# Optimization experiments

Measured on AMD Instinct MI355X. Metric: run time of the kernel, lower is better.

Reference implementation:

```python
import jax, jax.numpy as jnp
import numpy as np

B, C, H, W = 32, 256, 32, 32
HEADS, DH = 8, 32          # MHA9: num_heads=8, dim_head=32, total_dim=256
TOT = HEADS * DH


def setup_inputs() -> dict:
    key = jax.random.key(0)
    ks = jax.random.split(key, 10)
    s = 0.02
    return {
        "x": jax.random.normal(ks[0], (B, C, H, W), dtype=jnp.float32),
        "Wq": jax.random.normal(ks[1], (TOT, C), dtype=jnp.float32) * s,
        "bq": jnp.zeros((TOT,), dtype=jnp.float32),
        "Wk": jax.random.normal(ks[2], (TOT, C), dtype=jnp.float32) * s,
        "bk": jnp.zeros((TOT,), dtype=jnp.float32),
        "Wv": jax.random.normal(ks[3], (TOT, C), dtype=jnp.float32) * s,
        "bv": jnp.zeros((TOT,), dtype=jnp.float32),
        "Wo": jax.random.normal(ks[4], (C, TOT), dtype=jnp.float32) * s,
        "bo": jnp.zeros((C,), dtype=jnp.float32),
        "gamma": jnp.zeros((1,), dtype=jnp.float32),
    }


def reference(x, Wq, bq, Wk, bk, Wv, bv, Wo, bo, gamma):
    b, c, h, w = x.shape
    S = h * w

    def proj(Wt, bt):
        # 1x1 conv == channel matmul; reshape to (B, heads, S, dh)
        y = jnp.einsum('oc,bchw->bohw', Wt, x) + bt[None, :, None, None]
        return y.reshape(b, HEADS, DH, S).transpose(0, 1, 3, 2)

    q = proj(Wq, bq)
    k = proj(Wk, bk)
    v = proj(Wv, bv)

    scale = 1.0 / jnp.sqrt(jnp.asarray(DH, dtype=x.dtype))
    scores = jnp.einsum('bhsd,bhtd->bhst', q, k) * scale  # [B,h,S,S] full matrix
    weights = jax.nn.softmax(scores, axis=-1)
    o = jnp.einsum('bhst,bhtd->bhsd', weights, v)          # [B,h,S,dh]
    o = o.transpose(0, 1, 3, 2).reshape(b, TOT, h, w)
    o = jnp.einsum('oc,bchw->bohw', Wo, o) + bo[None, :, None, None]
    x_ = gamma * o + x   # inner residual of MultiHeadAttention
    return x + x_        # outer residual of MulAttontion
```

## Files before the change

### kernel.cpp

```cpp
#include <hip/hip_runtime.h>
#include <stdint.h>

typedef unsigned short u16;
typedef unsigned int   u32;
typedef __attribute__((ext_vector_type(8))) short bf16x8;
typedef __attribute__((ext_vector_type(4))) short bf16x4;
typedef __attribute__((ext_vector_type(4))) float f32x4;
typedef __attribute__((ext_vector_type(16))) float f32x16;

#define NT ((size_t)8388608)

__device__ __forceinline__ float bf2f(u16 u) {
  union { float f; u32 i; } v; v.i = ((u32)u) << 16; return v.f;
}
__device__ __forceinline__ u16 f2bf(float f) {
  union { float f; u32 i; } v; v.f = f;
  u32 r = (v.i + 0x7fffu + ((v.i >> 16) & 1u)) >> 16;
  return (u16)r;
}
__device__ __forceinline__ u32 fbits(float f) {
  union { float f; u32 i; } v; v.f = f; return v.i;
}
__device__ __forceinline__ int detect_bf16(const u32* __restrict__ xd) {
  u32 w = xd[threadIdx.x & 63];
  u32 e = (w >> 8) & 0x7fu;
  unsigned long long m = __ballot((e >= 0x38u) && (e <= 0x41u));
  return __popcll(m) > 32;
}
__device__ __forceinline__ void gld16(const void* g, void* l) {
  __builtin_amdgcn_global_load_lds((const __attribute__((address_space(1))) u32*)g,
                                   (__attribute__((address_space(3))) u32*)l, 16, 0, 0);
}

__global__ void __launch_bounds__(256) prologue_kernel(const void* __restrict__ xin,
                                                       u16* __restrict__ xT,
                                                       const void* __restrict__ W0, const void* __restrict__ W1,
                                                       const void* __restrict__ W2, const void* __restrict__ b0,
                                                       const void* __restrict__ b1, const void* __restrict__ b2,
                                                       u16* __restrict__ wdst, float* __restrict__ bdst,
                                                       const void* __restrict__ Wo, const void* __restrict__ bo,
                                                       const void* __restrict__ gm, u16* __restrict__ wodst,
                                                       float* __restrict__ bodst) {
  const int blk = blockIdx.x;
  const int tid = threadIdx.x;
  const int isbf = detect_bf16((const u32*)xin);
  if (blk < 2048) {
    const int s0 = (blk & 15) * 64, c0 = ((blk >> 4) & 3) * 64, b = blk >> 6;
    __shared__ u16 T[64][72];
    if (isbf) {
      const u16* xp = (const u16*)xin;
      for (int t = tid; t < 512; t += 256) {
        int r = t >> 3, off = (t & 7) * 8;
        *(uint4*)&T[r][off] = *(const uint4*)(xp + ((size_t)(b * 256 + c0 + r)) * 1024 + s0 + off);
      }
    } else {
      const float* xp = (const float*)xin;
      for (int t = tid; t < 512; t += 256) {
        int r = t >> 3, off = (t & 7) * 8;
        const float* s = xp + ((size_t)(b * 256 + c0 + r)) * 1024 + s0 + off;
#pragma unroll
        for (int u = 0; u < 8; u++) T[r][off + u] = f2bf(s[u]);
      }
    }
    __syncthreads();
    for (int t = tid; t < 512; t += 256) {
      int r = t >> 3, off = (t & 7) * 8;
      union { u16 h[8]; uint4 v; } pk;
#pragma unroll
      for (int u = 0; u < 8; u++) pk.h[u] = T[off + u][r];
      *(uint4*)(xT + ((size_t)(b * 1024 + s0 + r)) * 256 + c0 + off) = pk.v;
    }
  } else if (blk < 2240) {
    const int g = blk - 2048;
    const int which = g >> 6, bk = g & 63;
    const void* Ws = which == 0 ? W0 : which == 1 ? W1 : W2;
    const void* bs = which == 0 ? b0 : which == 1 ? b1 : b2;
    const int idx = bk * 1024 + tid * 4;
    u16* dst = wdst + which * 65536 + idx;
    if (isbf) {
      *(ushort4*)dst = *(const ushort4*)((const u16*)Ws + idx);
    } else {
      const float* s = (const float*)Ws + idx;
      ushort4 o; o.x = f2bf(s[0]); o.y = f2bf(s[1]); o.z = f2bf(s[2]); o.w = f2bf(s[3]);
      *(ushort4*)dst = o;
    }
    if (bk == 0) {
      bdst[which * 256 + tid] = isbf ? bf2f(((const u16*)bs)[tid]) : ((const float*)bs)[tid];
    }
  } else {
    const int g = blk - 2240;
    const int idx = g * 1024 + tid * 4;
    if (isbf) {
      *(ushort4*)(wodst + idx) = *(const ushort4*)((const u16*)Wo + idx);
    } else {
      const float* s = (const float*)Wo + idx;
      ushort4 o; o.x = f2bf(s[0]); o.y = f2bf(s[1]); o.z = f2bf(s[2]); o.w = f2bf(s[3]);
      *(ushort4*)(wodst + idx) = o;
    }
    if (g == 0) {
      bodst[tid] = isbf ? bf2f(((const u16*)bo)[tid]) : ((const float*)bo)[tid];
      if (tid == 0) bodst[256] = isbf ? bf2f(((const u16*)gm)[0]) : ((const float*)gm)[0];
    }
  }
}

__global__ void __launch_bounds__(256) prep_o(const void* __restrict__ Wo, const void* __restrict__ bo,
                                              const void* __restrict__ gm, u16* __restrict__ wdst,
                                              float* __restrict__ bdst, const u32* __restrict__ xdet) {
  const int isbf = detect_bf16(xdet);
  const int idx = blockIdx.x * 1024 + threadIdx.x * 4;
  if (isbf) {
    *(ushort4*)(wdst + idx) = *(const ushort4*)((const u16*)Wo + idx);
  } else {
    const float* s = (const float*)Wo + idx;
    ushort4 o; o.x = f2bf(s[0]); o.y = f2bf(s[1]); o.z = f2bf(s[2]); o.w = f2bf(s[3]);
    *(ushort4*)(wdst + idx) = o;
  }
  if (blockIdx.x == 0) {
    int t = threadIdx.x;
    bdst[t] = isbf ? bf2f(((const u16*)bo)[t]) : ((const float*)bo)[t];
    if (t == 0) bdst[256] = isbf ? bf2f(((const u16*)gm)[0]) : ((const float*)gm)[0];
  }
}

__global__ void __launch_bounds__(256) qkv_gemm(const u16* __restrict__ xT,
                                                const u16* __restrict__ Wall,
                                                const float* __restrict__ ball,
                                                u16* __restrict__ Qb, u16* __restrict__ Kb,
                                                u16* __restrict__ Vb) {
  const int z = blockIdx.z, b = z / 3, which = z - b * 3;
  const int tid = threadIdx.x, lane = tid & 63, wave = tid >> 6;
  const int quad = lane >> 4, l16 = lane & 15;
  const int wm = wave >> 1, wn = wave & 1;
  const u16* xb = xT + (size_t)b * 262144;
  const u16* W = Wall + which * 65536;
  int m0, n0; const u16 *Abase, *Bbase;
  if (which < 2) { m0 = blockIdx.y * 128; n0 = blockIdx.x * 128; Abase = xb; Bbase = W; }
  else           { m0 = blockIdx.x * 128; n0 = blockIdx.y * 128; Abase = W; Bbase = xb; }

  __shared__ u16 Ash[8192], Bsh[8192];
  f32x4 acc[4][4];
#pragma unroll
  for (int i = 0; i < 4; i++)
#pragma unroll
    for (int j = 0; j < 4; j++) acc[i][j] = (f32x4){0.f, 0.f, 0.f, 0.f};

  const int srow = lane >> 3, scol = (lane & 7) * 8;
  for (int k0 = 0; k0 < 256; k0 += 64) {
    __syncthreads();
#pragma unroll
    for (int p = 0; p < 4; p++) {
      const int row = p * 32 + wave * 8;
      gld16(Abase + (size_t)(m0 + row + srow) * 256 + k0 + scol, &Ash[row * 64 + lane * 8]);
      gld16(Bbase + (size_t)(n0 + row + srow) * 256 + k0 + scol, &Bsh[row * 64 + lane * 8]);
    }
    __syncthreads();
#pragma unroll
    for (int kk = 0; kk < 2; kk++) {
      bf16x8 av[4], bv[4];
#pragma unroll
      for (int i = 0; i < 4; i++) av[i] = *(const bf16x8*)&Ash[(wm * 64 + i * 16 + l16) * 64 + kk * 32 + quad * 8];
#pragma unroll
      for (int j = 0; j < 4; j++) bv[j] = *(const bf16x8*)&Bsh[(wn * 64 + j * 16 + l16) * 64 + kk * 32 + quad * 8];
#pragma unroll
      for (int i = 0; i < 4; i++)
#pragma unroll
        for (int j = 0; j < 4; j++)
          acc[i][j] = __builtin_amdgcn_mfma_f32_16x16x32_bf16(av[i], bv[j], acc[i][j], 0, 0, 0);
    }
  }

  const float* bias = ball + which * 256;
  const float scale = (which == 0) ? 0.25503486f : 1.0f;
#pragma unroll
  for (int i = 0; i < 4; i++) {
#pragma unroll
    for (int j = 0; j < 4; j++) {
      const int mb = m0 + wm * 64 + i * 16 + quad * 4;
      const int n = n0 + wn * 64 + j * 16 + l16;
#pragma unroll
      for (int r = 0; r < 4; r++) {
        const int m = mb + r;
        float v = acc[i][j][r];
        if (which < 2) {
          v = (v + bias[n]) * scale;
          u16* D = (which ? Kb : Qb) + (size_t)b * 262144;
          D[(size_t)m * 256 + n] = f2bf(v);
        } else {
          v = v + bias[m];
          (Vb + (size_t)b * 262144)[(size_t)m * 1024 + n] = f2bf(v);
        }
      }
    }
  }
}

__global__ void __launch_bounds__(512, 4) attn_kernel(const u16* __restrict__ Q,
                                                      const u16* __restrict__ K,
                                                      const u16* __restrict__ V,
                                                      u16* __restrict__ O) {
  const int blk = blockIdx.x;
  const int qc = blk >> 8, bh = blk & 255;
  const int b = bh >> 3, h = bh & 7;
  const int tid = threadIdx.x, wave = tid >> 6, lane = tid & 63;
  const int hi = lane >> 5, l32 = lane & 31;
  __shared__ __align__(16) u16 Ksh[2][128 * 32];
  __shared__ __align__(16) u16 Vsh[2][32 * 128];
  const u16* Qg = Q + (size_t)b * 262144 + h * 32;
  const u16* Kg = K + (size_t)b * 262144 + h * 32;
  const u16* Vg = V + (size_t)b * 262144 + (size_t)h * 32768;
  const int qw = qc * 256 + wave * 32;

  bf16x8 qf[2];
#pragma unroll
  for (int ks = 0; ks < 2; ks++)
    qf[ks] = *(const bf16x8*)(Qg + (size_t)(qw + l32) * 256 + ks * 16 + hi * 8);

  const int Gg = wave * 64 + lane;
  const int th = Gg >> 3;
  const int uu = (Gg & 7) ^ (th & 7);
  const u16* ksrc = Kg + (size_t)(th * 2 + (uu >> 2)) * 256 + (uu & 3) * 8;
  u16* kdst0 = &Ksh[0][Gg * 8];
  u16* kdst1 = &Ksh[1][Gg * 8];
  const int vd = tid >> 4;
  const u16* vsrc = Vg + (size_t)vd * 1024 + ((tid & 15) ^ (vd & 15)) * 8;
  u16* vdst0 = &Vsh[0][tid * 8];
  u16* vdst1 = &Vsh[1][tid * 8];

  const int kkey = (l32 >> 1) & 7;
  const int kb0 = (l32 >> 1) * 128 + (((((l32 & 1) << 2) | 0 | hi) ^ kkey) << 4);
  const int kb1 = (l32 >> 1) * 128 + (((((l32 & 1) << 2) | 2 | hi) ^ kkey) << 4);
  int vb[4];
#pragma unroll
  for (int tt = 0; tt < 4; tt++) vb[tt] = l32 * 256 + (((l32 & 12) ^ (tt << 2)) << 4);
  const int vm0 = ((l32 & 3) ^ hi) << 4;
  const int vm1 = ((l32 & 3) ^ (2 | hi)) << 4;

  f32x16 oacc;
#pragma unroll
  for (int r = 0; r < 16; r++) oacc[r] = 0.f;
  float lsum = 0.f;

  gld16(ksrc, kdst0);
  gld16(vsrc, vdst0);
  __syncthreads();

#pragma unroll 1
  for (int kt = 0; kt < 8; kt++) {
    const int c = kt & 1;
    if (kt < 7) {
      gld16(ksrc + (size_t)(kt + 1) * 32768, c ? kdst0 : kdst1);
      gld16(vsrc + (kt + 1) * 128,           c ? vdst0 : vdst1);
    }
    const char* Kb = (const char*)&Ksh[c][0];
    const char* Vb = (const char*)&Vsh[c][0];
#pragma unroll
    for (int tt = 0; tt < 4; tt++) {
      const bf16x8 kf0 = *(const bf16x8*)(Kb + tt * 2048 + kb0);
      const bf16x8 kf1 = *(const bf16x8*)(Kb + tt * 2048 + kb1);
      const bf16x8 vf0 = *(const bf16x8*)(Vb + vb[tt] + vm0);
      const bf16x8 vf1 = *(const bf16x8*)(Vb + vb[tt] + vm1);
      f32x16 sf;
#pragma unroll
      for (int r = 0; r < 16; r++) sf[r] = 0.f;
      __builtin_amdgcn_s_setprio(1);
      sf = __builtin_amdgcn_mfma_f32_32x32x16_bf16(kf0, qf[0], sf, 0, 0, 0);
      sf = __builtin_amdgcn_mfma_f32_32x32x16_bf16(kf1, qf[1], sf, 0, 0, 0);
      __builtin_amdgcn_s_setprio(0);
      {
        const float p0 = __builtin_amdgcn_exp2f(sf[0]);
        const float p1 = __builtin_amdgcn_exp2f(sf[1]);
        const float p2 = __builtin_amdgcn_exp2f(sf[2]);
        const float p3 = __builtin_amdgcn_exp2f(sf[3]);
        const float p4 = __builtin_amdgcn_exp2f(sf[4]);
        const float p5 = __builtin_amdgcn_exp2f(sf[5]);
        const float p6 = __builtin_amdgcn_exp2f(sf[6]);
        const float p7 = __builtin_amdgcn_exp2f(sf[7]);
        lsum += ((p0 + p1) + (p2 + p3)) + ((p4 + p5) + (p6 + p7));
        u32 wa, wb, wc, wd;
        asm("v_cvt_pk_bf16_f32 %0, %1, %2" : "=v"(wa) : "v"(p0), "v"(p1));
        asm("v_cvt_pk_bf16_f32 %0, %1, %2" : "=v"(wb) : "v"(p2), "v"(p3));
        asm("v_cvt_pk_bf16_f32 %0, %1, %2" : "=v"(wc) : "v"(p4), "v"(p5));
        asm("v_cvt_pk_bf16_f32 %0, %1, %2" : "=v"(wd) : "v"(p6), "v"(p7));
#if __has_builtin(__builtin_amdgcn_permlane32_swap)
        auto s0 = __builtin_amdgcn_permlane32_swap((int)wc, (int)wa, false, false);
        auto s1 = __builtin_amdgcn_permlane32_swap((int)wd, (int)wb, false, false);
        union { int w[4]; bf16x8 v; } pk;
        pk.w[0] = s0[1]; pk.w[1] = s1[1]; pk.w[2] = s0[0]; pk.w[3] = s1[0];
#else
        const u32 xa = __shfl_xor((int)wa, 32), xb = __shfl_xor((int)wb, 32);
        const u32 xc = __shfl_xor((int)wc, 32), xd = __shfl_xor((int)wd, 32);
        union { u32 w[4]; bf16x8 v; } pk;
        pk.w[0] = hi ? xc : wa; pk.w[1] = hi ? xd : wb;
        pk.w[2] = hi ? wc : xa; pk.w[3] = hi ? wd : xb;
#endif
        __builtin_amdgcn_s_setprio(1);
        oacc = __builtin_amdgcn_mfma_f32_32x32x16_bf16(pk.v, vf0, oacc, 0, 0, 0);
        __builtin_amdgcn_s_setprio(0);
      }
      {
        const float p0 = __builtin_amdgcn_exp2f(sf[8]);
        const float p1 = __builtin_amdgcn_exp2f(sf[9]);
        const float p2 = __builtin_amdgcn_exp2f(sf[10]);
        const float p3 = __builtin_amdgcn_exp2f(sf[11]);
        const float p4 = __builtin_amdgcn_exp2f(sf[12]);
        const float p5 = __builtin_amdgcn_exp2f(sf[13]);
        const float p6 = __builtin_amdgcn_exp2f(sf[14]);
        const float p7 = __builtin_amdgcn_exp2f(sf[15]);
        lsum += ((p0 + p1) + (p2 + p3)) + ((p4 + p5) + (p6 + p7));
        u32 wa, wb, wc, wd;
        asm("v_cvt_pk_bf16_f32 %0, %1, %2" : "=v"(wa) : "v"(p0), "v"(p1));
        asm("v_cvt_pk_bf16_f32 %0, %1, %2" : "=v"(wb) : "v"(p2), "v"(p3));
        asm("v_cvt_pk_bf16_f32 %0, %1, %2" : "=v"(wc) : "v"(p4), "v"(p5));
        asm("v_cvt_pk_bf16_f32 %0, %1, %2" : "=v"(wd) : "v"(p6), "v"(p7));
#if __has_builtin(__builtin_amdgcn_permlane32_swap)
        auto s0 = __builtin_amdgcn_permlane32_swap((int)wc, (int)wa, false, false);
        auto s1 = __builtin_amdgcn_permlane32_swap((int)wd, (int)wb, false, false);
        union { int w[4]; bf16x8 v; } pk;
        pk.w[0] = s0[1]; pk.w[1] = s1[1]; pk.w[2] = s0[0]; pk.w[3] = s1[0];
#else
        const u32 xa = __shfl_xor((int)wa, 32), xb = __shfl_xor((int)wb, 32);
        const u32 xc = __shfl_xor((int)wc, 32), xd = __shfl_xor((int)wd, 32);
        union { u32 w[4]; bf16x8 v; } pk;
        pk.w[0] = hi ? xc : wa; pk.w[1] = hi ? xd : wb;
        pk.w[2] = hi ? wc : xa; pk.w[3] = hi ? wd : xb;
#endif
        __builtin_amdgcn_s_setprio(1);
        oacc = __builtin_amdgcn_mfma_f32_32x32x16_bf16(pk.v, vf1, oacc, 0, 0, 0);
        __builtin_amdgcn_s_setprio(0);
      }
    }
    if (kt < 7) __syncthreads();
  }

  lsum += __shfl_xor(lsum, 32);
  const float linv = 1.0f / lsum;
  u16* Og = O + (size_t)(b * 1024 + qw) * 256 + h * 32 + l32;
#pragma unroll
  for (int r = 0; r < 16; r++) {
    const int qo = (r & 3) + 8 * (r >> 2) + 4 * hi;
    const float li = __shfl(linv, qo);
    Og[(size_t)qo * 256] = f2bf(oacc[r] * li);
  }
}

__global__ void __launch_bounds__(256) out_gemm(const u16* __restrict__ WoB,
                                                const float* __restrict__ bg,
                                                const u16* __restrict__ Ob,
                                                const void* __restrict__ xin,
                                                void* __restrict__ outp,
                                                const u32* __restrict__ xdet) {
  const int b = blockIdx.z;
  const int m0 = blockIdx.y * 128, n0 = blockIdx.x * 128;
  const int tid = threadIdx.x, lane = tid & 63, wave = tid >> 6;
  const int quad = lane >> 4, l16 = lane & 15;
  const int wm = wave >> 1, wn = wave & 1;
  const int isbf = detect_bf16(xdet);
  const u16* Bb = Ob + (size_t)b * 262144;
  __shared__ u16 Ash[8192], Bsh[8192];
  f32x4 acc[4][4];
#pragma unroll
  for (int i = 0; i < 4; i++)
#pragma unroll
    for (int j = 0; j < 4; j++) acc[i][j] = (f32x4){0.f, 0.f, 0.f, 0.f};

  const int srow = lane >> 3, scol = (lane & 7) * 8;
  for (int k0 = 0; k0 < 256; k0 += 64) {
    __syncthreads();
#pragma unroll
    for (int p = 0; p < 4; p++) {
      const int row = p * 32 + wave * 8;
      gld16(WoB + (size_t)(m0 + row + srow) * 256 + k0 + scol, &Ash[row * 64 + lane * 8]);
      gld16(Bb  + (size_t)(n0 + row + srow) * 256 + k0 + scol, &Bsh[row * 64 + lane * 8]);
    }
    __syncthreads();
#pragma unroll
    for (int kk = 0; kk < 2; kk++) {
      bf16x8 av[4], bv[4];
#pragma unroll
      for (int i = 0; i < 4; i++) av[i] = *(const bf16x8*)&Ash[(wm * 64 + i * 16 + l16) * 64 + kk * 32 + quad * 8];
#pragma unroll
      for (int j = 0; j < 4; j++) bv[j] = *(const bf16x8*)&Bsh[(wn * 64 + j * 16 + l16) * 64 + kk * 32 + quad * 8];
#pragma unroll
      for (int i = 0; i < 4; i++)
#pragma unroll
        for (int j = 0; j < 4; j++)
          acc[i][j] = __builtin_amdgcn_mfma_f32_16x16x32_bf16(av[i], bv[j], acc[i][j], 0, 0, 0);
    }
  }

  const float g = bg[256];
#pragma unroll
  for (int i = 0; i < 4; i++) {
#pragma unroll
    for (int j = 0; j < 4; j++) {
      const int mb = m0 + wm * 64 + i * 16 + quad * 4;
      const int n = n0 + wn * 64 + j * 16 + l16;
#pragma unroll
      for (int r = 0; r < 4; r++) {
        const int m = mb + r;
        const float v = acc[i][j][r] + bg[m];
        const size_t gi = (size_t)b * 262144 + (size_t)m * 1024 + n;
        const float xv = isbf ? bf2f(((const u16*)xin)[gi]) : ((const float*)xin)[gi];
        const float res = 2.f * xv + g * v;
        if (isbf) ((u16*)outp)[gi] = f2bf(res);
        else      ((float*)outp)[gi] = res;
      }
    }
  }
}

extern "C" void kernel_launch(void* const* d_in, const int* in_sizes, int n_in,
                              void* d_out, int out_size, void* d_ws, size_t ws_size,
                              hipStream_t stream) {
  const void* x  = d_in[0];
  const void* Wq = d_in[1]; const void* bq = d_in[2];
  const void* Wk = d_in[3]; const void* bk = d_in[4];
  const void* Wv = d_in[5]; const void* bv = d_in[6];
  const void* Wo = d_in[7]; const void* bo = d_in[8];
  const void* gm = d_in[9];

  u16* ws = (u16*)d_ws;
  u16* xT = ws;
  u16* Qb = ws + NT;
  u16* Kb = ws + 2 * NT;
  u16* Vb = ws + 3 * NT;
  u16* Ob = xT;
  const u32* xdet = (const u32*)x;

  u16* WqkvB = (u16*)d_out;
  float* bqkvF = (float*)((u16*)d_out + 196608);

  const bool tail = ws_size >= (size_t)(4 * NT + 66048) * 2;
  u16* WoB = tail ? (ws + 4 * NT) : Qb;
  float* boF = tail ? (float*)(ws + 4 * NT + 65536) : (float*)(Qb + 65536);

  prologue_kernel<<<dim3(tail ? 2304 : 2240), 256, 0, stream>>>(
      x, xT, Wq, Wk, Wv, bq, bk, bv, WqkvB, bqkvF, Wo, bo, gm, WoB, boF);
  qkv_gemm<<<dim3(2, 8, 96), 256, 0, stream>>>(xT, WqkvB, bqkvF, Qb, Kb, Vb);
  attn_kernel<<<dim3(1024), 512, 0, stream>>>(Qb, Kb, Vb, Ob);
  if (!tail) prep_o<<<dim3(64), 256, 0, stream>>>(Wo, bo, gm, WoB, boF, xdet);
  out_gemm<<<dim3(8, 2, 32), 256, 0, stream>>>(WoB, boF, Ob, x, d_out, xdet);
}
```

Before: 210.5 us.

## Swizzle GEMM LDS tiles, shrink out_gemm M-tile, pin attention waves per EU

Applies an XOR swizzle to the LDS column groups in both qkv_gemm and out_gemm so the 16-byte MFMA operand reads avoid bank conflicts. out_gemm's M tile is halved from 128 to 64, doubling its grid for more parallelism on the 256-CU device at the cost of more B-tile reloads. The attention kernel now sets occupancy through the amdgpu_waves_per_eu(4,4) attribute, and its per-iteration zero-init of the score accumulator is replaced by a hoisted zero vector.

```diff
diff --git a/kernel.cpp b/kernel.cpp
--- a/kernel.cpp
+++ b/kernel.cpp
@@ -145,23 +145,25 @@
 #pragma unroll
     for (int j = 0; j < 4; j++) acc[i][j] = (f32x4){0.f, 0.f, 0.f, 0.f};
 
-  const int srow = lane >> 3, scol = (lane & 7) * 8;
+  const int srow = lane >> 3;
+  const int sgc = (lane & 7) ^ (srow & 7);
   for (int k0 = 0; k0 < 256; k0 += 64) {
     __syncthreads();
 #pragma unroll
     for (int p = 0; p < 4; p++) {
       const int row = p * 32 + wave * 8;
-      gld16(Abase + (size_t)(m0 + row + srow) * 256 + k0 + scol, &Ash[row * 64 + lane * 8]);
-      gld16(Bbase + (size_t)(n0 + row + srow) * 256 + k0 + scol, &Bsh[row * 64 + lane * 8]);
+      gld16(Abase + (size_t)(m0 + row + srow) * 256 + k0 + sgc * 8, &Ash[row * 64 + lane * 8]);
+      gld16(Bbase + (size_t)(n0 + row + srow) * 256 + k0 + sgc * 8, &Bsh[row * 64 + lane * 8]);
     }
     __syncthreads();
 #pragma unroll
     for (int kk = 0; kk < 2; kk++) {
       bf16x8 av[4], bv[4];
-#pragma unroll
-      for (int i = 0; i < 4; i++) av[i] = *(const bf16x8*)&Ash[(wm * 64 + i * 16 + l16) * 64 + kk * 32 + quad * 8];
-#pragma unroll
-      for (int j = 0; j < 4; j++) bv[j] = *(const bf16x8*)&Bsh[(wn * 64 + j * 16 + l16) * 64 + kk * 32 + quad * 8];
+      const int rg = (kk * 4 + quad) ^ (l16 & 7);
+#pragma unroll
+      for (int i = 0; i < 4; i++) av[i] = *(const bf16x8*)&Ash[(wm * 64 + i * 16 + l16) * 64 + rg * 8];
+#pragma unroll
+      for (int j = 0; j < 4; j++) bv[j] = *(const bf16x8*)&Bsh[(wn * 64 + j * 16 + l16) * 64 + rg * 8];
 #pragma unroll
       for (int i = 0; i < 4; i++)
 #pragma unroll
@@ -195,10 +197,12 @@
   }
 }
 
-__global__ void __launch_bounds__(512, 4) attn_kernel(const u16* __restrict__ Q,
-                                                      const u16* __restrict__ K,
-                                                      const u16* __restrict__ V,
-                                                      u16* __restrict__ O) {
+__global__ void __launch_bounds__(512)
+__attribute__((amdgpu_waves_per_eu(4, 4)))
+attn_kernel(const u16* __restrict__ Q,
+            const u16* __restrict__ K,
+            const u16* __restrict__ V,
+            u16* __restrict__ O) {
   const int blk = blockIdx.x;
   const int qc = blk >> 8, bh = blk & 255;
   const int b = bh >> 3, h = bh & 7;
@@ -239,6 +243,9 @@
   f32x16 oacc;
 #pragma unroll
   for (int r = 0; r < 16; r++) oacc[r] = 0.f;
+  f32x16 zro;
+#pragma unroll
+  for (int r = 0; r < 16; r++) zro[r] = 0.f;
   float lsum = 0.f;
 
   gld16(ksrc, kdst0);
@@ -260,11 +267,8 @@
       const bf16x8 kf1 = *(const bf16x8*)(Kb + tt * 2048 + kb1);
       const bf16x8 vf0 = *(const bf16x8*)(Vb + vb[tt] + vm0);
       const bf16x8 vf1 = *(const bf16x8*)(Vb + vb[tt] + vm1);
-      f32x16 sf;
-#pragma unroll
-      for (int r = 0; r < 16; r++) sf[r] = 0.f;
       __builtin_amdgcn_s_setprio(1);
-      sf = __builtin_amdgcn_mfma_f32_32x32x16_bf16(kf0, qf[0], sf, 0, 0, 0);
+      f32x16 sf = __builtin_amdgcn_mfma_f32_32x32x16_bf16(kf0, qf[0], zro, 0, 0, 0);
       sf = __builtin_amdgcn_mfma_f32_32x32x16_bf16(kf1, qf[1], sf, 0, 0, 0);
       __builtin_amdgcn_s_setprio(0);
       {
@@ -351,38 +355,44 @@
                                                 void* __restrict__ outp,
                                                 const u32* __restrict__ xdet) {
   const int b = blockIdx.z;
-  const int m0 = blockIdx.y * 128, n0 = blockIdx.x * 128;
+  const int m0 = blockIdx.y * 64, n0 = blockIdx.x * 128;
   const int tid = threadIdx.x, lane = tid & 63, wave = tid >> 6;
   const int quad = lane >> 4, l16 = lane & 15;
   const int wm = wave >> 1, wn = wave & 1;
   const int isbf = detect_bf16(xdet);
   const u16* Bb = Ob + (size_t)b * 262144;
-  __shared__ u16 Ash[8192], Bsh[8192];
-  f32x4 acc[4][4];
-#pragma unroll
-  for (int i = 0; i < 4; i++)
+  __shared__ u16 Ash[4096], Bsh[8192];
+  f32x4 acc[2][4];
+#pragma unroll
+  for (int i = 0; i < 2; i++)
 #pragma unroll
     for (int j = 0; j < 4; j++) acc[i][j] = (f32x4){0.f, 0.f, 0.f, 0.f};
 
-  const int srow = lane >> 3, scol = (lane & 7) * 8;
+  const int srow = lane >> 3;
+  const int sgc = (lane & 7) ^ (srow & 7);
   for (int k0 = 0; k0 < 256; k0 += 64) {
     __syncthreads();
 #pragma unroll
+    for (int p = 0; p < 2; p++) {
+      const int row = p * 32 + wave * 8;
+      gld16(WoB + (size_t)(m0 + row + srow) * 256 + k0 + sgc * 8, &Ash[row * 64 + lane * 8]);
+    }
+#pragma unroll
     for (int p = 0; p < 4; p++) {
       const int row = p * 32 + wave * 8;
-      gld16(WoB + (size_t)(m0 + row + srow) * 256 + k0 + scol, &Ash[row * 64 + lane * 8]);
-      gld16(Bb  + (size_t)(n0 + row + srow) * 256 + k0 + scol, &Bsh[row * 64 + lane * 8]);
+      gld16(Bb + (size_t)(n0 + row + srow) * 256 + k0 + sgc * 8, &Bsh[row * 64 + lane * 8]);
     }
     __syncthreads();
 #pragma unroll
     for (int kk = 0; kk < 2; kk++) {
-      bf16x8 av[4], bv[4];
-#pragma unroll
-      for (int i = 0; i < 4; i++) av[i] = *(const bf16x8*)&Ash[(wm * 64 + i * 16 + l16) * 64 + kk * 32 + quad * 8];
-#pragma unroll
-      for (int j = 0; j < 4; j++) bv[j] = *(const bf16x8*)&Bsh[(wn * 64 + j * 16 + l16) * 64 + kk * 32 + quad * 8];
-#pragma unroll
-      for (int i = 0; i < 4; i++)
+      bf16x8 av[2], bv[4];
+      const int rg = (kk * 4 + quad) ^ (l16 & 7);
+#pragma unroll
+      for (int i = 0; i < 2; i++) av[i] = *(const bf16x8*)&Ash[(wm * 32 + i * 16 + l16) * 64 + rg * 8];
+#pragma unroll
+      for (int j = 0; j < 4; j++) bv[j] = *(const bf16x8*)&Bsh[(wn * 64 + j * 16 + l16) * 64 + rg * 8];
+#pragma unroll
+      for (int i = 0; i < 2; i++)
 #pragma unroll
         for (int j = 0; j < 4; j++)
           acc[i][j] = __builtin_amdgcn_mfma_f32_16x16x32_bf16(av[i], bv[j], acc[i][j], 0, 0, 0);
@@ -391,10 +401,10 @@
 
   const float g = bg[256];
 #pragma unroll
-  for (int i = 0; i < 4; i++) {
+  for (int i = 0; i < 2; i++) {
 #pragma unroll
     for (int j = 0; j < 4; j++) {
-      const int mb = m0 + wm * 64 + i * 16 + quad * 4;
+      const int mb = m0 + wm * 32 + i * 16 + quad * 4;
       const int n = n0 + wn * 64 + j * 16 + l16;
 #pragma unroll
       for (int r = 0; r < 4; r++) {
@@ -440,5 +450,5 @@
   qkv_gemm<<<dim3(2, 8, 96), 256, 0, stream>>>(xT, WqkvB, bqkvF, Qb, Kb, Vb);
   attn_kernel<<<dim3(1024), 512, 0, stream>>>(Qb, Kb, Vb, Ob);
   if (!tail) prep_o<<<dim3(64), 256, 0, stream>>>(Wo, bo, gm, WoB, boF, xdet);
-  out_gemm<<<dim3(8, 2, 32), 256, 0, stream>>>(WoB, boF, Ob, x, d_out, xdet);
-}
+  out_gemm<<<dim3(8, 4, 32), 256, 0, stream>>>(WoB, boF, Ob, x, d_out, xdet);
+}
```

New measurement: 202.7 us. 3.7% less time.
